# Kernel tuning notes

Hardware: AMD Instinct MI355X
Metric: run time of the kernel (lower is better)

## Reference

```python
import jax, jax.numpy as jnp
import numpy as np

NUM_ITEMS = 1_000_000
EMBED_DIM = 128
BATCH, SEQ = 16, 256
NUM_NEG = 256
TEMP = 0.05
EPS = 1e-12


def _l2norm(x):
    # F.normalize(p=2, dim=-1) with eps=1e-12
    n = jnp.sqrt(jnp.sum(x * x, axis=-1, keepdims=True))
    return x / jnp.maximum(n, EPS)


def setup_inputs() -> dict:
    key = jax.random.key(0)
    k1, k2, k3, k4, k5, k6 = jax.random.split(key, 6)
    output_embeddings = jax.random.normal(k1, (BATCH, SEQ, EMBED_DIM), jnp.float32)
    all_item_embeddings = jax.random.normal(k2, (NUM_ITEMS + 1, EMBED_DIM), jnp.float32)
    target_ids = jax.random.randint(k3, (BATCH, SEQ), 1, NUM_ITEMS + 1, jnp.int32)
    w = jax.random.uniform(k4, (BATCH, SEQ), jnp.float32)
    supervision_weights = jnp.where(w > 0.2, w, 0.0)
    N = BATCH * SEQ
    # negatives sampled uniformly in [1, num_items]; resample once on collision with target
    neg1 = jax.random.randint(k5, (N, NUM_NEG), 1, NUM_ITEMS + 1, jnp.int32)
    neg2 = jax.random.randint(k6, (N, NUM_NEG), 1, NUM_ITEMS + 1, jnp.int32)
    flat_t = target_ids.reshape(-1)
    neg_item_ids = jnp.where(neg1 != flat_t[:, None], neg1, neg2)
    return {
        "output_embeddings": output_embeddings,
        "all_item_embeddings": all_item_embeddings,
        "supervision_weights": supervision_weights,
        "target_ids": target_ids,
        "neg_item_ids": neg_item_ids,
    }


def reference(output_embeddings, all_item_embeddings, supervision_weights,
              target_ids, neg_item_ids):
    B, S, D = output_embeddings.shape
    max_item_idx = all_item_embeddings.shape[0] - 1  # = num_items

    flat_out = output_embeddings.reshape(-1, D)           # [N, D]
    flat_t = target_ids.reshape(-1)                       # [N]
    flat_w = supervision_weights.reshape(-1)              # [N]

    # instead of compacting valid rows, compute everywhere and weight by w
    # (w == 0 on invalid rows, so the weighted mean is identical)
    tgt_idx = jnp.clip(flat_t - 1, 0, max_item_idx)       # [N]

    q = _l2norm(flat_out)                                  # [N, D]
    norm_table = _l2norm(all_item_embeddings)              # full-table normalize (faithful)

    pos_emb = norm_table[tgt_idx]                          # [N, D]
    pos_logits = jnp.sum(q * pos_emb, axis=1, keepdims=True)  # [N, 1]

    neg_idx = jnp.clip(neg_item_ids - 1, 0, max_item_idx)  # [N, K]
    neg_emb = norm_table[neg_idx]                          # [N, K, D]
    neg_logits = jnp.einsum('nd,nkd->nk', q, neg_emb)      # [N, K]

    logits = jnp.concatenate([pos_logits, neg_logits], axis=1) / TEMP  # [N, 1+K]
    # cross-entropy with label 0
    loss_per = jax.nn.logsumexp(logits, axis=1) - logits[:, 0]          # [N]

    return jnp.sum(loss_per * flat_w) / jnp.sum(flat_w)
```

## Files before the change

### kernel.cpp

```cpp
#include <hip/hip_runtime.h>
#include <math.h>

#define DIMS 128
#define KNEG 256
#define INV_TEMP 20.0f
#define EPSN 1e-12f

__global__ __launch_bounds__(256, 8) void ssl_row_kernel(
    const float* __restrict__ out_emb,
    const float* __restrict__ table,
    const float* __restrict__ w,
    const int*   __restrict__ tgt,
    const int*   __restrict__ negs,
    float*       __restrict__ loss_out,
    int max_row)
{
    const int n = blockIdx.x;
    const int t = threadIdx.x;

    __shared__ __align__(16) float q_lds[DIMS];
    __shared__ float logits[KNEG + 1];
    __shared__ int   nid[KNEG];
    __shared__ float red[8];

    const float wn = w[n];
    if (wn == 0.0f) {
        if (t == 0) loss_out[n] = 0.0f;
        return;
    }

    float x = 0.0f;
    if (t < DIMS) x = out_emb[(size_t)n * DIMS + t];
    float ss = x * x;
    #pragma unroll
    for (int m = 1; m < 64; m <<= 1) ss += __shfl_xor(ss, m, 64);
    if ((t & 63) == 0) red[t >> 6] = ss;
    if (t < KNEG) nid[t] = negs[(size_t)n * KNEG + t];
    __syncthreads();
    const float inv_qn = 1.0f / fmaxf(sqrtf(red[0] + red[1]), EPSN);
    if (t < DIMS) q_lds[t] = x * inv_qn;
    __syncthreads();

    const int hw   = t >> 5;
    const int lane = t & 31;
    const float4 qv = *(const float4*)(q_lds + lane * 4);
    const int tgtn = tgt[n];

    auto rowp = [&](int id) -> const float4* {
        int i = id - 1; i = i < 0 ? 0 : (i > max_row ? max_row : i);
        return (const float4*)(table + (size_t)i * DIMS);
    };

    auto red_store = [&](float4 a, float4 b, int j) {
        float dq1 = qv.x*a.x + qv.y*a.y + qv.z*a.z + qv.w*a.w;
        float de1 = a.x*a.x + a.y*a.y + a.z*a.z + a.w*a.w;
        float dq2 = qv.x*b.x + qv.y*b.y + qv.z*b.z + qv.w*b.w;
        float de2 = b.x*b.x + b.y*b.y + b.z*b.z + b.w*b.w;
        #pragma unroll
        for (int m = 1; m < 32; m <<= 1) {
            dq1 += __shfl_xor(dq1, m, 64);
            de1 += __shfl_xor(de1, m, 64);
            dq2 += __shfl_xor(dq2, m, 64);
            de2 += __shfl_xor(de2, m, 64);
        }
        if (lane == 0) {
            logits[j]     = dq1 / fmaxf(sqrtf(de1), EPSN) * INV_TEMP;
            logits[j + 8] = dq2 / fmaxf(sqrtf(de2), EPSN) * INV_TEMP;
        }
    };

    float4 et;
    if (hw == 0) et = rowp(nid[KNEG - 1])[lane];

    #pragma unroll
    for (int p = 0; p < 16; ++p) {
        const int j1  = hw + (p << 4);
        const int id1 = (p == 0 && hw == 0) ? tgtn : nid[j1 - 1];
        const int id2 = nid[j1 + 7];
        const float4 a = rowp(id1)[lane];
        const float4 b = rowp(id2)[lane];
        red_store(a, b, j1);
    }

    if (hw == 0) {
        float dq1 = qv.x*et.x + qv.y*et.y + qv.z*et.z + qv.w*et.w;
        float de1 = et.x*et.x + et.y*et.y + et.z*et.z + et.w*et.w;
        #pragma unroll
        for (int m = 1; m < 32; m <<= 1) {
            dq1 += __shfl_xor(dq1, m, 64);
            de1 += __shfl_xor(de1, m, 64);
        }
        if (lane == 0) logits[KNEG] = dq1 / fmaxf(sqrtf(de1), EPSN) * INV_TEMP;
    }
    __syncthreads();

    float mx = logits[t];
    if (t == 0) mx = fmaxf(mx, logits[KNEG]);
    #pragma unroll
    for (int m = 1; m < 64; m <<= 1) mx = fmaxf(mx, __shfl_xor(mx, m, 64));
    if ((t & 63) == 0) red[t >> 6] = mx;
    __syncthreads();
    if (t == 0) red[4] = fmaxf(fmaxf(red[0], red[1]), fmaxf(red[2], red[3]));
    __syncthreads();
    mx = red[4];

    float p = expf(logits[t] - mx);
    if (t == 0) p += expf(logits[KNEG] - mx);
    #pragma unroll
    for (int m = 1; m < 64; m <<= 1) p += __shfl_xor(p, m, 64);
    if ((t & 63) == 0) red[t >> 6] = p;
    __syncthreads();
    if (t == 0) {
        const float s   = red[0] + red[1] + red[2] + red[3];
        const float lse = mx + logf(s);
        loss_out[n] = (lse - logits[0]) * wn;
    }
}

__global__ __launch_bounds__(256) void ssl_reduce_kernel(
    const float* __restrict__ loss,
    const float* __restrict__ w,
    float* __restrict__ out, int n)
{
    __shared__ float red[8];
    const int t = threadIdx.x;
    float sl = 0.0f, sw = 0.0f;
    for (int i = t; i < n; i += 256) { sl += loss[i]; sw += w[i]; }
    #pragma unroll
    for (int m = 1; m < 64; m <<= 1) {
        sl += __shfl_xor(sl, m, 64);
        sw += __shfl_xor(sw, m, 64);
    }
    if ((t & 63) == 0) { red[t >> 6] = sl; red[4 + (t >> 6)] = sw; }
    __syncthreads();
    if (t == 0) {
        const float SL = red[0] + red[1] + red[2] + red[3];
        const float SW = red[4] + red[5] + red[6] + red[7];
        out[0] = SL / SW;
    }
}

extern "C" void kernel_launch(void* const* d_in, const int* in_sizes, int n_in,
                              void* d_out, int out_size, void* d_ws, size_t ws_size,
                              hipStream_t stream) {
    const float* out_emb = (const float*)d_in[0];
    const float* table   = (const float*)d_in[1];
    const float* w       = (const float*)d_in[2];
    const int*   tgt     = (const int*)d_in[3];
    const int*   negs    = (const int*)d_in[4];

    const int N = in_sizes[2];
    const int rows = in_sizes[1] / DIMS;
    const int max_row = rows - 1;

    float* loss_ws = (float*)d_ws;

    ssl_row_kernel<<<N, 256, 0, stream>>>(out_emb, table, w, tgt, negs, loss_ws, max_row);
    ssl_reduce_kernel<<<1, 256, 0, stream>>>(loss_ws, w, (float*)d_out, N);
}
```

Baseline: 85.16 us.

## Fuse final reduction into row kernel via last-block atomic counter

Merges the per-row loss kernel and the single-block reduction kernel into one launch. Blocks bump a global counter after finishing, and the last block to arrive does the final weighted mean. A hipMemsetAsync resets the counter each call. The shuffle reduction is also reorganised: after two butterfly steps, the four partial sums are packed into quarter-wave groups and reduced together, which cuts the shuffle count per pair of rows. The grid still has one block per row, so the grid-stride loop runs once per block. In exchange it adds a memset and an atomic with fences.

After: 243.6 us. +186.1%, slower.

```diff
diff --git a/kernel.cpp b/kernel.cpp
--- a/kernel.cpp
+++ b/kernel.cpp
@@ -6,137 +6,140 @@
 #define INV_TEMP 20.0f
 #define EPSN 1e-12f
 
-__global__ __launch_bounds__(256, 8) void ssl_row_kernel(
+__global__ __launch_bounds__(256, 8) void ssl_fused_kernel(
     const float* __restrict__ out_emb,
     const float* __restrict__ table,
     const float* __restrict__ w,
     const int*   __restrict__ tgt,
     const int*   __restrict__ negs,
-    float*       __restrict__ loss_out,
-    int max_row)
+    float*       __restrict__ loss_ws,
+    unsigned*    __restrict__ cnt,
+    float*       __restrict__ out,
+    int N, int max_row)
 {
-    const int n = blockIdx.x;
-    const int t = threadIdx.x;
+    const int t    = threadIdx.x;
+    const int hw   = t >> 5;
+    const int lane = t & 31;
 
     __shared__ __align__(16) float q_lds[DIMS];
     __shared__ float logits[KNEG + 1];
     __shared__ int   nid[KNEG];
     __shared__ float red[8];
+    __shared__ unsigned sh_order;
 
-    const float wn = w[n];
-    if (wn == 0.0f) {
-        if (t == 0) loss_out[n] = 0.0f;
-        return;
+    for (int n = blockIdx.x; n < N; n += gridDim.x) {
+        const float wn = w[n];
+        if (wn == 0.0f) {
+            if (t == 0) loss_ws[n] = 0.0f;
+            continue;
+        }
+
+        float x = (t < DIMS) ? out_emb[(size_t)n * DIMS + t] : 0.0f;
+        float ss = x * x;
+        #pragma unroll
+        for (int m = 1; m < 64; m <<= 1) ss += __shfl_xor(ss, m, 64);
+        if ((t & 63) == 0) red[t >> 6] = ss;
+        nid[t] = negs[(size_t)n * KNEG + t];
+        __syncthreads();
+        const float inv_qn = 1.0f / fmaxf(sqrtf(red[0] + red[1]), EPSN);
+        if (t < DIMS) q_lds[t] = x * inv_qn;
+        __syncthreads();
+
+        const float4 qv = *(const float4*)(q_lds + lane * 4);
+        const int tgtn = tgt[n];
+
+        auto rowp = [&](int id) -> const float4* {
+            int i = id - 1; i = i < 0 ? 0 : (i > max_row ? max_row : i);
+            return (const float4*)(table + (size_t)i * DIMS);
+        };
+
+        float4 et;
+        if (hw == 0) et = rowp(nid[KNEG - 1])[lane];
+
+        #pragma unroll
+        for (int p = 0; p < 16; ++p) {
+            const int j1  = hw + (p << 4);
+            const int id1 = (p == 0 && hw == 0) ? tgtn : nid[j1 - 1];
+            const int id2 = nid[j1 + 7];
+            const float4 a = rowp(id1)[lane];
+            const float4 b = rowp(id2)[lane];
+            float dq1 = qv.x*a.x + qv.y*a.y + qv.z*a.z + qv.w*a.w;
+            float de1 = a.x*a.x + a.y*a.y + a.z*a.z + a.w*a.w;
+            float dq2 = qv.x*b.x + qv.y*b.y + qv.z*b.z + qv.w*b.w;
+            float de2 = b.x*b.x + b.y*b.y + b.z*b.z + b.w*b.w;
+            dq1 += __shfl_xor(dq1, 16, 64); de1 += __shfl_xor(de1, 16, 64);
+            dq2 += __shfl_xor(dq2, 16, 64); de2 += __shfl_xor(de2, 16, 64);
+            dq1 += __shfl_xor(dq1, 8, 64);  de1 += __shfl_xor(de1, 8, 64);
+            dq2 += __shfl_xor(dq2, 8, 64);  de2 += __shfl_xor(de2, 8, 64);
+            const int q = (lane >> 3) & 3;
+            float v = (q == 0) ? dq1 : (q == 1) ? de1 : (q == 2) ? dq2 : de2;
+            v += __shfl_xor(v, 1, 64);
+            v += __shfl_xor(v, 2, 64);
+            v += __shfl_xor(v, 4, 64);
+            const float u = __shfl_xor(v, 8, 64);
+            if (lane == 0)  logits[j1]     = v / fmaxf(sqrtf(u), EPSN) * INV_TEMP;
+            if (lane == 16) logits[j1 + 8] = v / fmaxf(sqrtf(u), EPSN) * INV_TEMP;
+        }
+
+        if (hw == 0) {
+            float dq = qv.x*et.x + qv.y*et.y + qv.z*et.z + qv.w*et.w;
+            float de = et.x*et.x + et.y*et.y + et.z*et.z + et.w*et.w;
+            dq += __shfl_xor(dq, 16, 64); de += __shfl_xor(de, 16, 64);
+            dq += __shfl_xor(dq, 8, 64);  de += __shfl_xor(de, 8, 64);
+            float v = (lane & 8) ? de : dq;
+            v += __shfl_xor(v, 1, 64);
+            v += __shfl_xor(v, 2, 64);
+            v += __shfl_xor(v, 4, 64);
+            const float u = __shfl_xor(v, 8, 64);
+            if (lane == 0) logits[KNEG] = v / fmaxf(sqrtf(u), EPSN) * INV_TEMP;
+        }
+        __syncthreads();
+
+        float mx = logits[t];
+        if (t == 0) mx = fmaxf(mx, logits[KNEG]);
+        #pragma unroll
+        for (int m = 1; m < 64; m <<= 1) mx = fmaxf(mx, __shfl_xor(mx, m, 64));
+        if ((t & 63) == 0) red[t >> 6] = mx;
+        __syncthreads();
+        if (t == 0) red[4] = fmaxf(fmaxf(red[0], red[1]), fmaxf(red[2], red[3]));
+        __syncthreads();
+        mx = red[4];
+
+        float pp = expf(logits[t] - mx);
+        if (t == 0) pp += expf(logits[KNEG] - mx);
+        #pragma unroll
+        for (int m = 1; m < 64; m <<= 1) pp += __shfl_xor(pp, m, 64);
+        if ((t & 63) == 0) red[t >> 6] = pp;
+        __syncthreads();
+        if (t == 0) {
+            const float s   = red[0] + red[1] + red[2] + red[3];
+            const float lse = mx + logf(s);
+            loss_ws[n] = (lse - logits[0]) * wn;
+        }
+        __syncthreads();
     }
 
-    float x = 0.0f;
-    if (t < DIMS) x = out_emb[(size_t)n * DIMS + t];
-    float ss = x * x;
-    #pragma unroll
-    for (int m = 1; m < 64; m <<= 1) ss += __shfl_xor(ss, m, 64);
-    if ((t & 63) == 0) red[t >> 6] = ss;
-    if (t < KNEG) nid[t] = negs[(size_t)n * KNEG + t];
-    __syncthreads();
-    const float inv_qn = 1.0f / fmaxf(sqrtf(red[0] + red[1]), EPSN);
-    if (t < DIMS) q_lds[t] = x * inv_qn;
-    __syncthreads();
-
-    const int hw   = t >> 5;
-    const int lane = t & 31;
-    const float4 qv = *(const float4*)(q_lds + lane * 4);
-    const int tgtn = tgt[n];
-
-    auto rowp = [&](int id) -> const float4* {
-        int i = id - 1; i = i < 0 ? 0 : (i > max_row ? max_row : i);
-        return (const float4*)(table + (size_t)i * DIMS);
-    };
-
-    auto red_store = [&](float4 a, float4 b, int j) {
-        float dq1 = qv.x*a.x + qv.y*a.y + qv.z*a.z + qv.w*a.w;
-        float de1 = a.x*a.x + a.y*a.y + a.z*a.z + a.w*a.w;
-        float dq2 = qv.x*b.x + qv.y*b.y + qv.z*b.z + qv.w*b.w;
-        float de2 = b.x*b.x + b.y*b.y + b.z*b.z + b.w*b.w;
-        #pragma unroll
-        for (int m = 1; m < 32; m <<= 1) {
-            dq1 += __shfl_xor(dq1, m, 64);
-            de1 += __shfl_xor(de1, m, 64);
-            dq2 += __shfl_xor(dq2, m, 64);
-            de2 += __shfl_xor(de2, m, 64);
-        }
-        if (lane == 0) {
-            logits[j]     = dq1 / fmaxf(sqrtf(de1), EPSN) * INV_TEMP;
-            logits[j + 8] = dq2 / fmaxf(sqrtf(de2), EPSN) * INV_TEMP;
-        }
-    };
-
-    float4 et;
-    if (hw == 0) et = rowp(nid[KNEG - 1])[lane];
-
-    #pragma unroll
-    for (int p = 0; p < 16; ++p) {
-        const int j1  = hw + (p << 4);
-        const int id1 = (p == 0 && hw == 0) ? tgtn : nid[j1 - 1];
-        const int id2 = nid[j1 + 7];
-        const float4 a = rowp(id1)[lane];
-        const float4 b = rowp(id2)[lane];
-        red_store(a, b, j1);
-    }
-
-    if (hw == 0) {
-        float dq1 = qv.x*et.x + qv.y*et.y + qv.z*et.z + qv.w*et.w;
-        float de1 = et.x*et.x + et.y*et.y + et.z*et.z + et.w*et.w;
-        #pragma unroll
-        for (int m = 1; m < 32; m <<= 1) {
-            dq1 += __shfl_xor(dq1, m, 64);
-            de1 += __shfl_xor(de1, m, 64);
-        }
-        if (lane == 0) logits[KNEG] = dq1 / fmaxf(sqrtf(de1), EPSN) * INV_TEMP;
+    if (t == 0) {
+        __threadfence();
+        sh_order = atomicAdd(cnt, 1u);
     }
     __syncthreads();
-
-    float mx = logits[t];
-    if (t == 0) mx = fmaxf(mx, logits[KNEG]);
-    #pragma unroll
-    for (int m = 1; m < 64; m <<= 1) mx = fmaxf(mx, __shfl_xor(mx, m, 64));
-    if ((t & 63) == 0) red[t >> 6] = mx;
-    __syncthreads();
-    if (t == 0) red[4] = fmaxf(fmaxf(red[0], red[1]), fmaxf(red[2], red[3]));
-    __syncthreads();
-    mx = red[4];
-
-    float p = expf(logits[t] - mx);
-    if (t == 0) p += expf(logits[KNEG] - mx);
-    #pragma unroll
-    for (int m = 1; m < 64; m <<= 1) p += __shfl_xor(p, m, 64);
-    if ((t & 63) == 0) red[t >> 6] = p;
-    __syncthreads();
-    if (t == 0) {
-        const float s   = red[0] + red[1] + red[2] + red[3];
-        const float lse = mx + logf(s);
-        loss_out[n] = (lse - logits[0]) * wn;
-    }
-}
-
-__global__ __launch_bounds__(256) void ssl_reduce_kernel(
-    const float* __restrict__ loss,
-    const float* __restrict__ w,
-    float* __restrict__ out, int n)
-{
-    __shared__ float red[8];
-    const int t = threadIdx.x;
-    float sl = 0.0f, sw = 0.0f;
-    for (int i = t; i < n; i += 256) { sl += loss[i]; sw += w[i]; }
-    #pragma unroll
-    for (int m = 1; m < 64; m <<= 1) {
-        sl += __shfl_xor(sl, m, 64);
-        sw += __shfl_xor(sw, m, 64);
-    }
-    if ((t & 63) == 0) { red[t >> 6] = sl; red[4 + (t >> 6)] = sw; }
-    __syncthreads();
-    if (t == 0) {
-        const float SL = red[0] + red[1] + red[2] + red[3];
-        const float SW = red[4] + red[5] + red[6] + red[7];
-        out[0] = SL / SW;
+    if (sh_order == (unsigned)(gridDim.x - 1)) {
+        __threadfence();
+        float sl = 0.0f, sw = 0.0f;
+        for (int i = t; i < N; i += 256) { sl += loss_ws[i]; sw += w[i]; }
+        #pragma unroll
+        for (int m = 1; m < 64; m <<= 1) {
+            sl += __shfl_xor(sl, m, 64);
+            sw += __shfl_xor(sw, m, 64);
+        }
+        if ((t & 63) == 0) { red[t >> 6] = sl; red[4 + (t >> 6)] = sw; }
+        __syncthreads();
+        if (t == 0) {
+            const float SL = red[0] + red[1] + red[2] + red[3];
+            const float SW = red[4] + red[5] + red[6] + red[7];
+            out[0] = SL / SW;
+        }
     }
 }
 
@@ -153,8 +156,11 @@
     const int rows = in_sizes[1] / DIMS;
     const int max_row = rows - 1;
 
-    float* loss_ws = (float*)d_ws;
+    unsigned* cnt  = (unsigned*)d_ws;
+    float* loss_ws = (float*)((char*)d_ws + 64);
 
-    ssl_row_kernel<<<N, 256, 0, stream>>>(out_emb, table, w, tgt, negs, loss_ws, max_row);
-    ssl_reduce_kernel<<<1, 256, 0, stream>>>(loss_ws, w, (float*)d_out, N);
+    hipMemsetAsync(cnt, 0, sizeof(unsigned), stream);
+    ssl_fused_kernel<<<N, 256, 0, stream>>>(out_emb, table, w, tgt, negs,
+                                            loss_ws, cnt, (float*)d_out,
+                                            N, max_row);
 }
```
